# Optimization experiments

Measured on AMD Instinct MI355X. Metric: run time of the kernel, lower is better.

## Reference

```python
import jax, jax.numpy as jnp
import numpy as np

N_NODES = 100_000
N_EDGES = 1_600_000
N_GRAPHS = 32
D_IN = 64
D_H1 = 64
D_H2 = 64
D_OUT = 10


def setup_inputs() -> dict:
    key = jax.random.key(0)
    ks = jax.random.split(key, 6)
    x = jax.random.normal(ks[0], (N_NODES, D_IN), dtype=jnp.float32)
    edge_index = jax.random.randint(ks[1], (2, N_EDGES), 0, N_NODES, dtype=jnp.int32)
    edge_weight = jax.random.uniform(ks[2], (N_EDGES,), dtype=jnp.float32)
    # deterministic sorted graph assignment: every one of the 32 graphs nonempty
    batch = ((jnp.arange(N_NODES) * N_GRAPHS) // N_NODES).astype(jnp.int32)
    W1 = jax.random.normal(ks[3], (D_IN, D_H1), dtype=jnp.float32) * 0.1
    b1 = jnp.zeros((D_H1,), dtype=jnp.float32)
    W2 = jax.random.normal(ks[4], (D_H1, D_H2), dtype=jnp.float32) * 0.1
    b2 = jnp.zeros((D_H2,), dtype=jnp.float32)
    Wlin = jax.random.normal(ks[5], (D_H2, D_OUT), dtype=jnp.float32) * 0.1
    blin = jnp.zeros((D_OUT,), dtype=jnp.float32)
    return {"x": x, "edge_index": edge_index, "edge_weight": edge_weight,
            "batch": batch, "W1": W1, "b1": b1, "W2": W2, "b2": b2,
            "Wlin": Wlin, "blin": blin}


def _gcn_norm(edge_index, edge_weight, n_nodes):
    """GCNConv(improved=True) normalization: add self-loops with weight 2.0,
    then norm_e = deg(dst)^-1/2 * w_e * deg(src)^-1/2."""
    loop = jnp.arange(n_nodes, dtype=edge_index.dtype)
    src = jnp.concatenate([edge_index[0], loop])
    dst = jnp.concatenate([edge_index[1], loop])
    w = jnp.concatenate([edge_weight, jnp.full((n_nodes,), 2.0, edge_weight.dtype)])
    deg = jax.ops.segment_sum(w, dst, num_segments=n_nodes)
    dinv = jnp.where(deg > 0, jax.lax.rsqrt(deg), 0.0)
    norm = dinv[src] * w * dinv[dst]
    return src, dst, norm


def _gcn_conv(h, W, b, src, dst, norm, n_nodes):
    hw = h @ W                                   # [N, d_out] transform first
    msg = hw[src] * norm[:, None]                # gather + scale  [E+N, d_out]
    return jax.ops.segment_sum(msg, dst, num_segments=n_nodes) + b


def reference(x, edge_index, edge_weight, batch, W1, b1, W2, b2, Wlin, blin):
    n = x.shape[0]
    src, dst, norm = _gcn_norm(edge_index, edge_weight, n)
    h = jax.nn.relu(_gcn_conv(x, W1, b1, src, dst, norm, n))
    h = jax.nn.relu(_gcn_conv(h, W2, b2, src, dst, norm, n))
    pooled = jax.ops.segment_max(h, batch, num_segments=N_GRAPHS)  # [G, d_h2]
    return pooled @ Wlin + blin
```

## Files before the change

### kernel.cpp

```cpp
#include <hip/hip_runtime.h>

#define N_NODES 100000
#define N_GRAPHS 32
#define N_EDGES 1600000
#define NODES_PER_GRAPH 3125
#define D 64
#define DOUT 10
#define CAP 64
#define PARTS 8
#define PART_NODES 12500
#define NCHUNK 782
#define CHUNK_EDGES 2048
#define EDGE_BLOCKS (PARTS * NCHUNK)
#define GEMM_BLOCKS 6250
#define WQ 32767.0f
#define POOL_SLICES 16

__device__ __forceinline__ unsigned short f2bf(float x) {
    unsigned u = __float_as_uint(x);
    u += 0x7FFFu + ((u >> 16) & 1u);
    return (unsigned short)(u >> 16);
}
__device__ __forceinline__ float bf2f(unsigned short h) {
    return __uint_as_float((unsigned)h << 16);
}
__device__ __forceinline__ float bflo(unsigned u) { return __uint_as_float(u << 16); }
__device__ __forceinline__ float bfhi(unsigned u) { return __uint_as_float(u & 0xFFFF0000u); }

__global__ void k_init(int* cnt, unsigned int* pooled) {
    int i = blockIdx.x * blockDim.x + threadIdx.x;
    if (i < N_NODES) cnt[i] = 0;
    if (i < N_GRAPHS * D) pooled[i] = 0u;
}

__global__ void k_fill_gemm(const int* __restrict__ src, const int* __restrict__ dst,
                            const float* __restrict__ w, int* cnt,
                            unsigned int* __restrict__ bucket,
                            const float* __restrict__ X, const float* __restrict__ W,
                            unsigned short* __restrict__ Y) {
    __shared__ float4 Ws[64 * 16];
    if (blockIdx.x < EDGE_BLOCKS) {
        int p = blockIdx.x & 7;
        int chunk = blockIdx.x >> 3;
        int base = chunk * CHUNK_EDGES;
        int lo = p * PART_NODES, hi = lo + PART_NODES;
#pragma unroll
        for (int j = 0; j < 8; ++j) {
            int e = base + j * 256 + threadIdx.x;
            if (e < N_EDGES) {
                int d = dst[e];
                if (d >= lo && d < hi) {
                    int pos = atomicAdd(&cnt[d], 1);
                    if (pos < CAP) {
                        unsigned int wq = (unsigned int)(w[e] * WQ + 0.5f);
                        bucket[d * CAP + pos] = ((unsigned int)src[e] << 15) | wq;
                    }
                }
            }
        }
    } else {
        int t = threadIdx.x;
        const float4* W4 = (const float4*)W;
        for (int i = t; i < 1024; i += 256) Ws[i] = W4[i];
        __syncthreads();
        int row = (blockIdx.x - EDGE_BLOCKS) * 16 + (t >> 4);
        int c4 = t & 15;
        const float4* xr4 = (const float4*)(X + (size_t)row * D);
        float4 acc = {0.f, 0.f, 0.f, 0.f};
#pragma unroll
        for (int k4 = 0; k4 < 16; ++k4) {
            float4 xv = xr4[k4];
            float4 w0 = Ws[(k4 * 4 + 0) * 16 + c4];
            float4 w1 = Ws[(k4 * 4 + 1) * 16 + c4];
            float4 w2 = Ws[(k4 * 4 + 2) * 16 + c4];
            float4 w3 = Ws[(k4 * 4 + 3) * 16 + c4];
            acc.x += xv.x * w0.x + xv.y * w1.x + xv.z * w2.x + xv.w * w3.x;
            acc.y += xv.x * w0.y + xv.y * w1.y + xv.z * w2.y + xv.w * w3.y;
            acc.z += xv.x * w0.z + xv.y * w1.z + xv.z * w2.z + xv.w * w3.z;
            acc.w += xv.x * w0.w + xv.y * w1.w + xv.z * w2.w + xv.w * w3.w;
        }
        ushort4 o;
        o.x = f2bf(acc.x); o.y = f2bf(acc.y); o.z = f2bf(acc.z); o.w = f2bf(acc.w);
        ((ushort4*)Y)[(size_t)row * 16 + c4] = o;
    }
}

__global__ void k_deg(const int* __restrict__ cnt, const unsigned int* __restrict__ bucket,
                      float* __restrict__ dinv) {
    int node = blockIdx.x * 4 + (threadIdx.x >> 6);
    int lane = threadIdx.x & 63;
    int c = cnt[node];
    if (c > CAP) c = CAP;
    float wv = 0.0f;
    if (lane < c) wv = (float)(bucket[node * CAP + lane] & 32767u);
#pragma unroll
    for (int off = 1; off < 64; off <<= 1) wv += __shfl_xor(wv, off);
    if (lane == 0) dinv[node] = rsqrtf(2.0f + wv * (1.0f / WQ));
}

__global__ void k_gemm64v(const float* __restrict__ X, const float* __restrict__ W,
                          unsigned short* __restrict__ Y) {
    __shared__ float4 Ws[64 * 16];
    int t = threadIdx.x;
    const float4* W4 = (const float4*)W;
    for (int i = t; i < 1024; i += 256) Ws[i] = W4[i];
    __syncthreads();
    int row = blockIdx.x * 16 + (t >> 4);
    int c4 = t & 15;
    const float4* xr4 = (const float4*)(X + (size_t)row * D);
    float4 acc = {0.f, 0.f, 0.f, 0.f};
#pragma unroll
    for (int k4 = 0; k4 < 16; ++k4) {
        float4 xv = xr4[k4];
        float4 w0 = Ws[(k4 * 4 + 0) * 16 + c4];
        float4 w1 = Ws[(k4 * 4 + 1) * 16 + c4];
        float4 w2 = Ws[(k4 * 4 + 2) * 16 + c4];
        float4 w3 = Ws[(k4 * 4 + 3) * 16 + c4];
        acc.x += xv.x * w0.x + xv.y * w1.x + xv.z * w2.x + xv.w * w3.x;
        acc.y += xv.x * w0.y + xv.y * w1.y + xv.z * w2.y + xv.w * w3.y;
        acc.z += xv.x * w0.z + xv.y * w1.z + xv.z * w2.z + xv.w * w3.z;
        acc.w += xv.x * w0.w + xv.y * w1.w + xv.z * w2.w + xv.w * w3.w;
    }
    ushort4 o;
    o.x = f2bf(acc.x); o.y = f2bf(acc.y); o.z = f2bf(acc.z); o.w = f2bf(acc.w);
    ((ushort4*)Y)[(size_t)row * 16 + c4] = o;
}

#define GATHER_BODY                                                              \
    int node = blockIdx.x * 4 + (threadIdx.x >> 6);                              \
    int lane = threadIdx.x & 63;                                                 \
    int g = lane >> 3, q = lane & 7;                                             \
    int end = cnt[node];                                                         \
    if (end > CAP) end = CAP;                                                    \
    float dvd = dinv[node];                                                      \
    float wsc = dvd * (1.0f / WQ);                                               \
    const unsigned int* bk = bucket + node * CAP;                                \
    float a0=0.f,a1=0.f,a2=0.f,a3=0.f,a4=0.f,a5=0.f,a6=0.f,a7=0.f;               \
    if (g == 0) {                                      \
        float s = 2.0f * dvd * dvd;                                              \
        uint4 u = hw8[(size_t)node * 8 + q];                                     \
        a0 = bflo(u.x)*s; a1 = bfhi(u.x)*s; a2 = bflo(u.y)*s; a3 = bfhi(u.y)*s;  \
        a4 = bflo(u.z)*s; a5 = bfhi(u.z)*s; a6 = bflo(u.w)*s; a7 = bfhi(u.w)*s;  \
    }                                                                            \
    int e = g;                                                                   \
    for (; e + 8 < end; e += 16) {                                               \
        unsigned int e0 = bk[e];                                                 \
        unsigned int e1 = bk[e + 8];                                             \
        int s0 = e0 >> 15, s1 = e1 >> 15;                                        \
        float d0 = dinv[s0], d1 = dinv[s1];                                      \
        uint4 u0 = hw8[(size_t)s0 * 8 + q];                                      \
        uint4 u1 = hw8[(size_t)s1 * 8 + q];                                      \
        float n0 = d0 * (float)(e0 & 32767u) * wsc;                              \
        float n1 = d1 * (float)(e1 & 32767u) * wsc;                              \
        a0 += bflo(u0.x)*n0 + bflo(u1.x)*n1; a1 += bfhi(u0.x)*n0 + bfhi(u1.x)*n1;\
        a2 += bflo(u0.y)*n0 + bflo(u1.y)*n1; a3 += bfhi(u0.y)*n0 + bfhi(u1.y)*n1;\
        a4 += bflo(u0.z)*n0 + bflo(u1.z)*n1; a5 += bfhi(u0.z)*n0 + bfhi(u1.z)*n1;\
        a6 += bflo(u0.w)*n0 + bflo(u1.w)*n1; a7 += bfhi(u0.w)*n0 + bfhi(u1.w)*n1;\
    }                                                                            \
    for (; e < end; e += 8) {                                                    \
        unsigned int ee = bk[e];                                                 \
        int s = ee >> 15;                                                        \
        float nrm = dinv[s] * (float)(ee & 32767u) * wsc;                        \
        uint4 u = hw8[(size_t)s * 8 + q];                                        \
        a0 += bflo(u.x)*nrm; a1 += bfhi(u.x)*nrm;                                \
        a2 += bflo(u.y)*nrm; a3 += bfhi(u.y)*nrm;                                \
        a4 += bflo(u.z)*nrm; a5 += bfhi(u.z)*nrm;                                \
        a6 += bflo(u.w)*nrm; a7 += bfhi(u.w)*nrm;                                \
    }                                                                            \
                            \
    a0 += __shfl_xor(a0, 8);  a1 += __shfl_xor(a1, 8);                           \
    a2 += __shfl_xor(a2, 8);  a3 += __shfl_xor(a3, 8);                           \
    a4 += __shfl_xor(a4, 8);  a5 += __shfl_xor(a5, 8);                           \
    a6 += __shfl_xor(a6, 8);  a7 += __shfl_xor(a7, 8);                           \
    a0 += __shfl_xor(a0, 16); a1 += __shfl_xor(a1, 16);                          \
    a2 += __shfl_xor(a2, 16); a3 += __shfl_xor(a3, 16);                          \
    a4 += __shfl_xor(a4, 16); a5 += __shfl_xor(a5, 16);                          \
    a6 += __shfl_xor(a6, 16); a7 += __shfl_xor(a7, 16);                          \
    a0 += __shfl_xor(a0, 32); a1 += __shfl_xor(a1, 32);                          \
    a2 += __shfl_xor(a2, 32); a3 += __shfl_xor(a3, 32);                          \
    a4 += __shfl_xor(a4, 32); a5 += __shfl_xor(a5, 32);                          \
    a6 += __shfl_xor(a6, 32); a7 += __shfl_xor(a7, 32);

__global__ void k_gather8_f32(const int* __restrict__ cnt, const unsigned int* __restrict__ bucket,
                              const uint4* __restrict__ hw8, const float* __restrict__ dinv,
                              const float* __restrict__ b, float4* __restrict__ out4) {
    GATHER_BODY
    if (g == 0) {
        float4 b0 = ((const float4*)b)[2 * q];
        float4 b1 = ((const float4*)b)[2 * q + 1];
        float4 r0, r1;
        r0.x = fmaxf(a0 + b0.x, 0.f); r0.y = fmaxf(a1 + b0.y, 0.f);
        r0.z = fmaxf(a2 + b0.z, 0.f); r0.w = fmaxf(a3 + b0.w, 0.f);
        r1.x = fmaxf(a4 + b1.x, 0.f); r1.y = fmaxf(a5 + b1.y, 0.f);
        r1.z = fmaxf(a6 + b1.z, 0.f); r1.w = fmaxf(a7 + b1.w, 0.f);
        out4[(size_t)node * 16 + 2 * q] = r0;
        out4[(size_t)node * 16 + 2 * q + 1] = r1;
    }
}

__global__ void k_gather8_bf16(const int* __restrict__ cnt, const unsigned int* __restrict__ bucket,
                               const uint4* __restrict__ hw8, const float* __restrict__ dinv,
                               const float* __restrict__ b, uint4* __restrict__ outb) {
    GATHER_BODY
    if (g == 0) {
        float4 b0 = ((const float4*)b)[2 * q];
        float4 b1 = ((const float4*)b)[2 * q + 1];
        uint4 r;
        r.x = (unsigned)f2bf(fmaxf(a0 + b0.x, 0.f)) | ((unsigned)f2bf(fmaxf(a1 + b0.y, 0.f)) << 16);
        r.y = (unsigned)f2bf(fmaxf(a2 + b0.z, 0.f)) | ((unsigned)f2bf(fmaxf(a3 + b0.w, 0.f)) << 16);
        r.z = (unsigned)f2bf(fmaxf(a4 + b1.x, 0.f)) | ((unsigned)f2bf(fmaxf(a5 + b1.y, 0.f)) << 16);
        r.w = (unsigned)f2bf(fmaxf(a6 + b1.z, 0.f)) | ((unsigned)f2bf(fmaxf(a7 + b1.w, 0.f)) << 16);
        outb[(size_t)node * 8 + q] = r;
    }
}

__global__ void k_pool(const unsigned short* __restrict__ h, unsigned int* pooled) {
    __shared__ float s[256];
    int g = blockIdx.x / POOL_SLICES;
    int slice = blockIdx.x % POOL_SLICES;
    int t = threadIdx.x;
    int f = t & 63, r = t >> 6;
    float m = 0.0f;
    size_t base = (size_t)g * NODES_PER_GRAPH;
    for (int i = slice * 4 + r; i < NODES_PER_GRAPH; i += 4 * POOL_SLICES)
        m = fmaxf(m, bf2f(h[(base + i) * D + f]));
    s[t] = m;
    __syncthreads();
    if (t < 128) s[t] = fmaxf(s[t], s[t + 128]);
    __syncthreads();
    if (t < 64) atomicMax(&pooled[g * D + t], __float_as_uint(fmaxf(s[t], s[t + 64])));
}

__global__ void k_final(const float* __restrict__ pooled, const float* __restrict__ Wlin,
                        const float* __restrict__ blin, float* __restrict__ out) {
    int t = threadIdx.x;
    if (t < N_GRAPHS * DOUT) {
        int g = t / DOUT, o = t % DOUT;
        float acc = blin[o];
#pragma unroll
        for (int f = 0; f < D; ++f) acc += pooled[g * D + f] * Wlin[f * DOUT + o];
        out[t] = acc;
    }
}

extern "C" void kernel_launch(void* const* d_in, const int* in_sizes, int n_in,
                              void* d_out, int out_size, void* d_ws, size_t ws_size,
                              hipStream_t stream) {
    const float* x     = (const float*)d_in[0];
    const int*   ei    = (const int*)d_in[1];
    const int*   src   = ei;
    const int*   dst   = ei + N_EDGES;
    const float* ew    = (const float*)d_in[2];
    const float* W1    = (const float*)d_in[4];
    const float* b1    = (const float*)d_in[5];
    const float* W2    = (const float*)d_in[6];
    const float* b2    = (const float*)d_in[7];
    const float* Wlin  = (const float*)d_in[8];
    const float* blin  = (const float*)d_in[9];
    float* out = (float*)d_out;

    unsigned int* bucket = (unsigned int*)d_ws;
    float* h1     = (float*)(bucket + (size_t)N_NODES * CAP);
    unsigned short* hwA = (unsigned short*)(h1 + (size_t)N_NODES * D);
    unsigned short* hwB = hwA + (size_t)N_NODES * D;
    unsigned short* h2  = hwB + (size_t)N_NODES * D;
    float* dinv   = (float*)(h2 + (size_t)N_NODES * D);
    float* pooled = dinv + N_NODES;
    int*   cnt    = (int*)(pooled + N_GRAPHS * D);

    const int B = 256;
    int gN = (N_NODES + B - 1) / B;

    k_init<<<gN, B, 0, stream>>>(cnt, (unsigned int*)pooled);
    k_fill_gemm<<<EDGE_BLOCKS + GEMM_BLOCKS, B, 0, stream>>>(src, dst, ew, cnt, bucket, x, W1, hwA);
    k_deg<<<N_NODES / 4, B, 0, stream>>>(cnt, bucket, dinv);

    k_gather8_f32<<<N_NODES / 4, B, 0, stream>>>(cnt, bucket, (const uint4*)hwA, dinv, b1, (float4*)h1);
    k_gemm64v<<<GEMM_BLOCKS, B, 0, stream>>>(h1, W2, hwB);
    k_gather8_bf16<<<N_NODES / 4, B, 0, stream>>>(cnt, bucket, (const uint4*)hwB, dinv, b2, (uint4*)h2);

    k_pool<<<N_GRAPHS * POOL_SLICES, B, 0, stream>>>(h2, (unsigned int*)pooled);
    k_final<<<1, 320, 0, stream>>>(pooled, Wlin, blin, out);
}
```

Before: 324.2 us.

## Store layer-1 output in bf16, swizzle node blocks, nontemporal loads, vectorize pooling

The first-layer gather now writes its activations as bf16 instead of fp32, and a new GEMM reads that bf16 input, roughly halving traffic for that intermediate. Node-indexed kernels use a swizzled block-to-node mapping that interleaves the node range across blocks. The edge-fill and first GEMM use nontemporal loads for streaming inputs. The pooling kernel reads two bf16 features per 32-bit load. In exchange, layer-1 activations carry bf16 rounding error.

```diff
diff --git a/kernel.cpp b/kernel.cpp
--- a/kernel.cpp
+++ b/kernel.cpp
@@ -15,6 +15,9 @@
 #define GEMM_BLOCKS 6250
 #define WQ 32767.0f
 #define POOL_SLICES 16
+#define NODE_BLOCKS 25000
+
+typedef float f32x4 __attribute__((ext_vector_type(4)));
 
 __device__ __forceinline__ unsigned short f2bf(float x) {
     unsigned u = __float_as_uint(x);
@@ -48,12 +51,14 @@
         for (int j = 0; j < 8; ++j) {
             int e = base + j * 256 + threadIdx.x;
             if (e < N_EDGES) {
-                int d = dst[e];
+                int d = __builtin_nontemporal_load(&dst[e]);
                 if (d >= lo && d < hi) {
                     int pos = atomicAdd(&cnt[d], 1);
                     if (pos < CAP) {
-                        unsigned int wq = (unsigned int)(w[e] * WQ + 0.5f);
-                        bucket[d * CAP + pos] = ((unsigned int)src[e] << 15) | wq;
+                        float wv = __builtin_nontemporal_load(&w[e]);
+                        int sv = __builtin_nontemporal_load(&src[e]);
+                        unsigned int wq = (unsigned int)(wv * WQ + 0.5f);
+                        bucket[d * CAP + pos] = ((unsigned int)sv << 15) | wq;
                     }
                 }
             }
@@ -65,11 +70,11 @@
         __syncthreads();
         int row = (blockIdx.x - EDGE_BLOCKS) * 16 + (t >> 4);
         int c4 = t & 15;
-        const float4* xr4 = (const float4*)(X + (size_t)row * D);
+        const f32x4* xr4 = (const f32x4*)(X + (size_t)row * D);
         float4 acc = {0.f, 0.f, 0.f, 0.f};
 #pragma unroll
         for (int k4 = 0; k4 < 16; ++k4) {
-            float4 xv = xr4[k4];
+            f32x4 xv = __builtin_nontemporal_load(&xr4[k4]);
             float4 w0 = Ws[(k4 * 4 + 0) * 16 + c4];
             float4 w1 = Ws[(k4 * 4 + 1) * 16 + c4];
             float4 w2 = Ws[(k4 * 4 + 2) * 16 + c4];
@@ -85,9 +90,13 @@
     }
 }
 
+__device__ __forceinline__ int swiz_node(int bidx, int tid) {
+    return ((bidx & 7) * (NODE_BLOCKS / 8) + (bidx >> 3)) * 4 + (tid >> 6);
+}
+
 __global__ void k_deg(const int* __restrict__ cnt, const unsigned int* __restrict__ bucket,
                       float* __restrict__ dinv) {
-    int node = blockIdx.x * 4 + (threadIdx.x >> 6);
+    int node = swiz_node(blockIdx.x, threadIdx.x);
     int lane = threadIdx.x & 63;
     int c = cnt[node];
     if (c > CAP) c = CAP;
@@ -98,110 +107,61 @@
     if (lane == 0) dinv[node] = rsqrtf(2.0f + wv * (1.0f / WQ));
 }
 
-__global__ void k_gemm64v(const float* __restrict__ X, const float* __restrict__ W,
-                          unsigned short* __restrict__ Y) {
-    __shared__ float4 Ws[64 * 16];
-    int t = threadIdx.x;
-    const float4* W4 = (const float4*)W;
-    for (int i = t; i < 1024; i += 256) Ws[i] = W4[i];
-    __syncthreads();
-    int row = blockIdx.x * 16 + (t >> 4);
-    int c4 = t & 15;
-    const float4* xr4 = (const float4*)(X + (size_t)row * D);
-    float4 acc = {0.f, 0.f, 0.f, 0.f};
-#pragma unroll
-    for (int k4 = 0; k4 < 16; ++k4) {
-        float4 xv = xr4[k4];
-        float4 w0 = Ws[(k4 * 4 + 0) * 16 + c4];
-        float4 w1 = Ws[(k4 * 4 + 1) * 16 + c4];
-        float4 w2 = Ws[(k4 * 4 + 2) * 16 + c4];
-        float4 w3 = Ws[(k4 * 4 + 3) * 16 + c4];
-        acc.x += xv.x * w0.x + xv.y * w1.x + xv.z * w2.x + xv.w * w3.x;
-        acc.y += xv.x * w0.y + xv.y * w1.y + xv.z * w2.y + xv.w * w3.y;
-        acc.z += xv.x * w0.z + xv.y * w1.z + xv.z * w2.z + xv.w * w3.z;
-        acc.w += xv.x * w0.w + xv.y * w1.w + xv.z * w2.w + xv.w * w3.w;
-    }
-    ushort4 o;
-    o.x = f2bf(acc.x); o.y = f2bf(acc.y); o.z = f2bf(acc.z); o.w = f2bf(acc.w);
-    ((ushort4*)Y)[(size_t)row * 16 + c4] = o;
-}
-
-#define GATHER_BODY                                                              \
-    int node = blockIdx.x * 4 + (threadIdx.x >> 6);                              \
-    int lane = threadIdx.x & 63;                                                 \
-    int g = lane >> 3, q = lane & 7;                                             \
-    int end = cnt[node];                                                         \
-    if (end > CAP) end = CAP;                                                    \
-    float dvd = dinv[node];                                                      \
-    float wsc = dvd * (1.0f / WQ);                                               \
-    const unsigned int* bk = bucket + node * CAP;                                \
-    float a0=0.f,a1=0.f,a2=0.f,a3=0.f,a4=0.f,a5=0.f,a6=0.f,a7=0.f;               \
-    if (g == 0) {                                      \
-        float s = 2.0f * dvd * dvd;                                              \
-        uint4 u = hw8[(size_t)node * 8 + q];                                     \
-        a0 = bflo(u.x)*s; a1 = bfhi(u.x)*s; a2 = bflo(u.y)*s; a3 = bfhi(u.y)*s;  \
-        a4 = bflo(u.z)*s; a5 = bfhi(u.z)*s; a6 = bflo(u.w)*s; a7 = bfhi(u.w)*s;  \
-    }                                                                            \
-    int e = g;                                                                   \
-    for (; e + 8 < end; e += 16) {                                               \
-        unsigned int e0 = bk[e];                                                 \
-        unsigned int e1 = bk[e + 8];                                             \
-        int s0 = e0 >> 15, s1 = e1 >> 15;                                        \
-        float d0 = dinv[s0], d1 = dinv[s1];                                      \
-        uint4 u0 = hw8[(size_t)s0 * 8 + q];                                      \
-        uint4 u1 = hw8[(size_t)s1 * 8 + q];                                      \
-        float n0 = d0 * (float)(e0 & 32767u) * wsc;                              \
-        float n1 = d1 * (float)(e1 & 32767u) * wsc;                              \
-        a0 += bflo(u0.x)*n0 + bflo(u1.x)*n1; a1 += bfhi(u0.x)*n0 + bfhi(u1.x)*n1;\
-        a2 += bflo(u0.y)*n0 + bflo(u1.y)*n1; a3 += bfhi(u0.y)*n0 + bfhi(u1.y)*n1;\
-        a4 += bflo(u0.z)*n0 + bflo(u1.z)*n1; a5 += bfhi(u0.z)*n0 + bfhi(u1.z)*n1;\
-        a6 += bflo(u0.w)*n0 + bflo(u1.w)*n1; a7 += bfhi(u0.w)*n0 + bfhi(u1.w)*n1;\
-    }                                                                            \
-    for (; e < end; e += 8) {                                                    \
-        unsigned int ee = bk[e];                                                 \
-        int s = ee >> 15;                                                        \
-        float nrm = dinv[s] * (float)(ee & 32767u) * wsc;                        \
-        uint4 u = hw8[(size_t)s * 8 + q];                                        \
-        a0 += bflo(u.x)*nrm; a1 += bfhi(u.x)*nrm;                                \
-        a2 += bflo(u.y)*nrm; a3 += bfhi(u.y)*nrm;                                \
-        a4 += bflo(u.z)*nrm; a5 += bfhi(u.z)*nrm;                                \
-        a6 += bflo(u.w)*nrm; a7 += bfhi(u.w)*nrm;                                \
-    }                                                                            \
-                            \
-    a0 += __shfl_xor(a0, 8);  a1 += __shfl_xor(a1, 8);                           \
-    a2 += __shfl_xor(a2, 8);  a3 += __shfl_xor(a3, 8);                           \
-    a4 += __shfl_xor(a4, 8);  a5 += __shfl_xor(a5, 8);                           \
-    a6 += __shfl_xor(a6, 8);  a7 += __shfl_xor(a7, 8);                           \
-    a0 += __shfl_xor(a0, 16); a1 += __shfl_xor(a1, 16);                          \
-    a2 += __shfl_xor(a2, 16); a3 += __shfl_xor(a3, 16);                          \
-    a4 += __shfl_xor(a4, 16); a5 += __shfl_xor(a5, 16);                          \
-    a6 += __shfl_xor(a6, 16); a7 += __shfl_xor(a7, 16);                          \
-    a0 += __shfl_xor(a0, 32); a1 += __shfl_xor(a1, 32);                          \
-    a2 += __shfl_xor(a2, 32); a3 += __shfl_xor(a3, 32);                          \
-    a4 += __shfl_xor(a4, 32); a5 += __shfl_xor(a5, 32);                          \
-    a6 += __shfl_xor(a6, 32); a7 += __shfl_xor(a7, 32);
-
-__global__ void k_gather8_f32(const int* __restrict__ cnt, const unsigned int* __restrict__ bucket,
-                              const uint4* __restrict__ hw8, const float* __restrict__ dinv,
-                              const float* __restrict__ b, float4* __restrict__ out4) {
-    GATHER_BODY
-    if (g == 0) {
-        float4 b0 = ((const float4*)b)[2 * q];
-        float4 b1 = ((const float4*)b)[2 * q + 1];
-        float4 r0, r1;
-        r0.x = fmaxf(a0 + b0.x, 0.f); r0.y = fmaxf(a1 + b0.y, 0.f);
-        r0.z = fmaxf(a2 + b0.z, 0.f); r0.w = fmaxf(a3 + b0.w, 0.f);
-        r1.x = fmaxf(a4 + b1.x, 0.f); r1.y = fmaxf(a5 + b1.y, 0.f);
-        r1.z = fmaxf(a6 + b1.z, 0.f); r1.w = fmaxf(a7 + b1.w, 0.f);
-        out4[(size_t)node * 16 + 2 * q] = r0;
-        out4[(size_t)node * 16 + 2 * q + 1] = r1;
-    }
-}
-
 __global__ void k_gather8_bf16(const int* __restrict__ cnt, const unsigned int* __restrict__ bucket,
                                const uint4* __restrict__ hw8, const float* __restrict__ dinv,
                                const float* __restrict__ b, uint4* __restrict__ outb) {
-    GATHER_BODY
+    int node = swiz_node(blockIdx.x, threadIdx.x);
+    int lane = threadIdx.x & 63;
+    int g = lane >> 3, q = lane & 7;
+    int end = cnt[node];
+    if (end > CAP) end = CAP;
+    float dvd = dinv[node];
+    float wsc = dvd * (1.0f / WQ);
+    const unsigned int* bk = bucket + node * CAP;
+    float a0=0.f,a1=0.f,a2=0.f,a3=0.f,a4=0.f,a5=0.f,a6=0.f,a7=0.f;
+    if (g == 0) {
+        float s = 2.0f * dvd * dvd;
+        uint4 u = hw8[(size_t)node * 8 + q];
+        a0 = bflo(u.x)*s; a1 = bfhi(u.x)*s; a2 = bflo(u.y)*s; a3 = bfhi(u.y)*s;
+        a4 = bflo(u.z)*s; a5 = bfhi(u.z)*s; a6 = bflo(u.w)*s; a7 = bfhi(u.w)*s;
+    }
+    int e = g;
+    for (; e + 8 < end; e += 16) {
+        unsigned int e0 = bk[e];
+        unsigned int e1 = bk[e + 8];
+        int s0 = e0 >> 15, s1 = e1 >> 15;
+        float d0 = dinv[s0], d1 = dinv[s1];
+        uint4 u0 = hw8[(size_t)s0 * 8 + q];
+        uint4 u1 = hw8[(size_t)s1 * 8 + q];
+        float n0 = d0 * (float)(e0 & 32767u) * wsc;
+        float n1 = d1 * (float)(e1 & 32767u) * wsc;
+        a0 += bflo(u0.x)*n0 + bflo(u1.x)*n1; a1 += bfhi(u0.x)*n0 + bfhi(u1.x)*n1;
+        a2 += bflo(u0.y)*n0 + bflo(u1.y)*n1; a3 += bfhi(u0.y)*n0 + bfhi(u1.y)*n1;
+        a4 += bflo(u0.z)*n0 + bflo(u1.z)*n1; a5 += bfhi(u0.z)*n0 + bfhi(u1.z)*n1;
+        a6 += bflo(u0.w)*n0 + bflo(u1.w)*n1; a7 += bfhi(u0.w)*n0 + bfhi(u1.w)*n1;
+    }
+    for (; e < end; e += 8) {
+        unsigned int ee = bk[e];
+        int s = ee >> 15;
+        float nrm = dinv[s] * (float)(ee & 32767u) * wsc;
+        uint4 u = hw8[(size_t)s * 8 + q];
+        a0 += bflo(u.x)*nrm; a1 += bfhi(u.x)*nrm;
+        a2 += bflo(u.y)*nrm; a3 += bfhi(u.y)*nrm;
+        a4 += bflo(u.z)*nrm; a5 += bfhi(u.z)*nrm;
+        a6 += bflo(u.w)*nrm; a7 += bfhi(u.w)*nrm;
+    }
+    a0 += __shfl_xor(a0, 8);  a1 += __shfl_xor(a1, 8);
+    a2 += __shfl_xor(a2, 8);  a3 += __shfl_xor(a3, 8);
+    a4 += __shfl_xor(a4, 8);  a5 += __shfl_xor(a5, 8);
+    a6 += __shfl_xor(a6, 8);  a7 += __shfl_xor(a7, 8);
+    a0 += __shfl_xor(a0, 16); a1 += __shfl_xor(a1, 16);
+    a2 += __shfl_xor(a2, 16); a3 += __shfl_xor(a3, 16);
+    a4 += __shfl_xor(a4, 16); a5 += __shfl_xor(a5, 16);
+    a6 += __shfl_xor(a6, 16); a7 += __shfl_xor(a7, 16);
+    a0 += __shfl_xor(a0, 32); a1 += __shfl_xor(a1, 32);
+    a2 += __shfl_xor(a2, 32); a3 += __shfl_xor(a3, 32);
+    a4 += __shfl_xor(a4, 32); a5 += __shfl_xor(a5, 32);
+    a6 += __shfl_xor(a6, 32); a7 += __shfl_xor(a7, 32);
     if (g == 0) {
         float4 b0 = ((const float4*)b)[2 * q];
         float4 b1 = ((const float4*)b)[2 * q + 1];
@@ -214,21 +174,64 @@
     }
 }
 
+__global__ void k_gemm64b(const unsigned short* __restrict__ Xb, const float* __restrict__ W,
+                          unsigned short* __restrict__ Y) {
+    __shared__ float4 Ws[64 * 16];
+    int t = threadIdx.x;
+    const float4* W4 = (const float4*)W;
+    for (int i = t; i < 1024; i += 256) Ws[i] = W4[i];
+    __syncthreads();
+    int row = blockIdx.x * 16 + (t >> 4);
+    int c4 = t & 15;
+    const uint4* xr = (const uint4*)(Xb + (size_t)row * D);
+    uint4 u8[8];
+#pragma unroll
+    for (int m = 0; m < 8; ++m) u8[m] = xr[m];
+    float4 acc = {0.f, 0.f, 0.f, 0.f};
+#pragma unroll
+    for (int k4 = 0; k4 < 16; ++k4) {
+        uint4 uu = u8[k4 >> 1];
+        unsigned ua = (k4 & 1) ? uu.z : uu.x;
+        unsigned ub = (k4 & 1) ? uu.w : uu.y;
+        float xv0 = bflo(ua), xv1 = bfhi(ua), xv2 = bflo(ub), xv3 = bfhi(ub);
+        float4 w0 = Ws[(k4 * 4 + 0) * 16 + c4];
+        float4 w1 = Ws[(k4 * 4 + 1) * 16 + c4];
+        float4 w2 = Ws[(k4 * 4 + 2) * 16 + c4];
+        float4 w3 = Ws[(k4 * 4 + 3) * 16 + c4];
+        acc.x += xv0 * w0.x + xv1 * w1.x + xv2 * w2.x + xv3 * w3.x;
+        acc.y += xv0 * w0.y + xv1 * w1.y + xv2 * w2.y + xv3 * w3.y;
+        acc.z += xv0 * w0.z + xv1 * w1.z + xv2 * w2.z + xv3 * w3.z;
+        acc.w += xv0 * w0.w + xv1 * w1.w + xv2 * w2.w + xv3 * w3.w;
+    }
+    ushort4 o;
+    o.x = f2bf(acc.x); o.y = f2bf(acc.y); o.z = f2bf(acc.z); o.w = f2bf(acc.w);
+    ((ushort4*)Y)[(size_t)row * 16 + c4] = o;
+}
+
 __global__ void k_pool(const unsigned short* __restrict__ h, unsigned int* pooled) {
-    __shared__ float s[256];
+    __shared__ float2 s[256];
     int g = blockIdx.x / POOL_SLICES;
     int slice = blockIdx.x % POOL_SLICES;
     int t = threadIdx.x;
-    int f = t & 63, r = t >> 6;
-    float m = 0.0f;
-    size_t base = (size_t)g * NODES_PER_GRAPH;
-    for (int i = slice * 4 + r; i < NODES_PER_GRAPH; i += 4 * POOL_SLICES)
-        m = fmaxf(m, bf2f(h[(base + i) * D + f]));
-    s[t] = m;
-    __syncthreads();
-    if (t < 128) s[t] = fmaxf(s[t], s[t + 128]);
-    __syncthreads();
-    if (t < 64) atomicMax(&pooled[g * D + t], __float_as_uint(fmaxf(s[t], s[t + 64])));
+    int f2 = t & 31;
+    int r = t >> 5;
+    float m0 = 0.0f, m1 = 0.0f;
+    const unsigned int* hu = (const unsigned int*)(h + (size_t)g * NODES_PER_GRAPH * D);
+    for (int i = slice * 8 + r; i < NODES_PER_GRAPH; i += 8 * POOL_SLICES) {
+        unsigned int u = hu[(size_t)i * 32 + f2];
+        m0 = fmaxf(m0, bflo(u));
+        m1 = fmaxf(m1, bfhi(u));
+    }
+    s[t].x = m0; s[t].y = m1;
+    __syncthreads();
+    if (t < 128) { s[t].x = fmaxf(s[t].x, s[t + 128].x); s[t].y = fmaxf(s[t].y, s[t + 128].y); }
+    __syncthreads();
+    if (t < 64)  { s[t].x = fmaxf(s[t].x, s[t + 64].x);  s[t].y = fmaxf(s[t].y, s[t + 64].y); }
+    __syncthreads();
+    if (t < 32) {
+        atomicMax(&pooled[g * D + 2 * t],     __float_as_uint(fmaxf(s[t].x, s[t + 32].x)));
+        atomicMax(&pooled[g * D + 2 * t + 1], __float_as_uint(fmaxf(s[t].y, s[t + 32].y)));
+    }
 }
 
 __global__ void k_final(const float* __restrict__ pooled, const float* __restrict__ Wlin,
@@ -260,9 +263,9 @@
     float* out = (float*)d_out;
 
     unsigned int* bucket = (unsigned int*)d_ws;
-    float* h1     = (float*)(bucket + (size_t)N_NODES * CAP);
-    unsigned short* hwA = (unsigned short*)(h1 + (size_t)N_NODES * D);
-    unsigned short* hwB = hwA + (size_t)N_NODES * D;
+    unsigned short* hwA = (unsigned short*)(bucket + (size_t)N_NODES * CAP);
+    unsigned short* h1b = hwA + (size_t)N_NODES * D;
+    unsigned short* hwB = h1b + (size_t)N_NODES * D;
     unsigned short* h2  = hwB + (size_t)N_NODES * D;
     float* dinv   = (float*)(h2 + (size_t)N_NODES * D);
     float* pooled = dinv + N_NODES;
@@ -273,11 +276,11 @@
 
     k_init<<<gN, B, 0, stream>>>(cnt, (unsigned int*)pooled);
     k_fill_gemm<<<EDGE_BLOCKS + GEMM_BLOCKS, B, 0, stream>>>(src, dst, ew, cnt, bucket, x, W1, hwA);
-    k_deg<<<N_NODES / 4, B, 0, stream>>>(cnt, bucket, dinv);
-
-    k_gather8_f32<<<N_NODES / 4, B, 0, stream>>>(cnt, bucket, (const uint4*)hwA, dinv, b1, (float4*)h1);
-    k_gemm64v<<<GEMM_BLOCKS, B, 0, stream>>>(h1, W2, hwB);
-    k_gather8_bf16<<<N_NODES / 4, B, 0, stream>>>(cnt, bucket, (const uint4*)hwB, dinv, b2, (uint4*)h2);
+    k_deg<<<NODE_BLOCKS, B, 0, stream>>>(cnt, bucket, dinv);
+
+    k_gather8_bf16<<<NODE_BLOCKS, B, 0, stream>>>(cnt, bucket, (const uint4*)hwA, dinv, b1, (uint4*)h1b);
+    k_gemm64b<<<GEMM_BLOCKS, B, 0, stream>>>(h1b, W2, hwB);
+    k_gather8_bf16<<<NODE_BLOCKS, B, 0, stream>>>(cnt, bucket, (const uint4*)hwB, dinv, b2, (uint4*)h2);
 
     k_pool<<<N_GRAPHS * POOL_SLICES, B, 0, stream>>>(h2, (unsigned int*)pooled);
     k_final<<<1, 320, 0, stream>>>(pooled, Wlin, blin, out);
```

After: 322.8 us, median of 2. No clear change (-0.4%).
